# Kernel optimization log

Hardware: AMD Instinct MI355X
Metric: run time of the kernel (lower is better)

Reference implementation:

```python
import jax, jax.numpy as jnp
import numpy as np

B, T, C, H = 4, 4096, 512, 64

def setup_inputs() -> dict:
    key = jax.random.key(0)
    ks = jax.random.split(key, 9)
    k = jax.random.normal(ks[0], (B, T, C), dtype=jnp.float32)
    v = jax.random.normal(ks[1], (B, T, C), dtype=jnp.float32)
    q = jax.random.normal(ks[2], (B, T, C), dtype=jnp.float32)
    # causal lower-triangular mask, positions with 0 are masked to -inf
    mask = jnp.tril(jnp.ones((T, T), dtype=jnp.int32))
    s = 1.0 / np.sqrt(C)
    kW = jax.random.normal(ks[3], (C, H), dtype=jnp.float32) * s
    kb = jax.random.normal(ks[4], (H,), dtype=jnp.float32) * s
    vW = jax.random.normal(ks[5], (C, H), dtype=jnp.float32) * s
    vb = jax.random.normal(ks[6], (H,), dtype=jnp.float32) * s
    qW = jax.random.normal(ks[7], (C, H), dtype=jnp.float32) * s
    qb = jax.random.normal(ks[8], (H,), dtype=jnp.float32) * s
    return {"k": k, "v": v, "q": q, "mask": mask,
            "kW": kW, "kb": kb, "vW": vW, "vb": vb, "qW": qW, "qb": qb}

def reference(k, v, q, mask, kW, kb, vW, vb, qW, qb):
    C_in = k.shape[-1]
    kp = k @ kW + kb                              # [B,T,H]
    qp = q @ qW + qb                              # [B,T,H]
    # NOTE: original scales by embedding_size**-0.5 (C), not head_size**-0.5
    attn = jnp.einsum('bth,bsh->bts', qp, kp) * (C_in ** -0.5)  # [B,T,T]
    attn = jnp.where(mask[None, :, :] == 0, -jnp.inf, attn)
    attn = jax.nn.softmax(attn, axis=-1)
    vp = v @ vW + vb                              # [B,T,H]
    out = attn @ vp                               # [B,T,H]
    return out
```

## Files before the change

kernel.cpp:

```cpp
#include <hip/hip_runtime.h>
#include <hip/hip_bf16.h>

#define Bq 4
#define Tq 4096
#define Cq 512
#define Hq 64
#define NEG_BIG (-3.0e38f)

using bf16   = __bf16;
using bf16x8 = __attribute__((ext_vector_type(8))) __bf16;
using bf16x4 = __attribute__((ext_vector_type(4))) __bf16;
using f32x4  = __attribute__((ext_vector_type(4))) float;
using f32x16 = __attribute__((ext_vector_type(16))) float;

static __device__ __forceinline__ float other_half_f(float x) {
    return __shfl_xor(x, 32, 64);
}
static __device__ __forceinline__ unsigned other_half_u(unsigned x) {
    return (unsigned)__shfl_xor((int)x, 32, 64);
}
static __device__ __forceinline__ unsigned pk2(float x, float y) {
    union { bf16 h[2]; unsigned u; } t;
    t.h[0] = (bf16)x; t.h[1] = (bf16)y;
    return t.u;
}
union W8 { unsigned u[4]; bf16x8 v; };

#define BUILD_B(p, BA, BB) do {                                                \
    const unsigned w0 = pk2(p[0],  p[1]),  w1 = pk2(p[2],  p[3]);              \
    const unsigned w2 = pk2(p[4],  p[5]),  w3 = pk2(p[6],  p[7]);              \
    const unsigned w4 = pk2(p[8],  p[9]),  w5 = pk2(p[10], p[11]);             \
    const unsigned w6 = pk2(p[12], p[13]), w7 = pk2(p[14], p[15]);             \
    const unsigned o0 = other_half_u(w0), o1 = other_half_u(w1);               \
    const unsigned o2 = other_half_u(w2), o3 = other_half_u(w3);               \
    const unsigned o4 = other_half_u(w4), o5 = other_half_u(w5);               \
    const unsigned o6 = other_half_u(w6), o7 = other_half_u(w7);               \
    BA.u[0] = hi ? o2 : w0;  BA.u[1] = hi ? o3 : w1;                           \
    BA.u[2] = hi ? w2 : o0;  BA.u[3] = hi ? w3 : o1;                           \
    BB.u[0] = hi ? o6 : w4;  BB.u[1] = hi ? o7 : w5;                           \
    BB.u[2] = hi ? w6 : o4;  BB.u[3] = hi ? w7 : o5;                           \
} while (0)

__global__ __launch_bounds__(256) void prep_weights_kernel(
    const float* __restrict__ kW, const float* __restrict__ qW,
    const float* __restrict__ vW, bf16* __restrict__ WT)
{
    int i = blockIdx.x * 256 + threadIdx.x;
    int t = i >> 15;
    int r = i & 32767;
    int c = r >> 6;
    int h = r & 63;
    const float* W = (t == 0) ? kW : (t == 1) ? qW : vW;
    WT[(size_t)t * 32768 + h * 512 + c] = (bf16)W[r];
}

__global__ __launch_bounds__(256, 2) void proj_kernel(
    const float* __restrict__ Xk, const float* __restrict__ Xq,
    const float* __restrict__ Xv, const bf16* __restrict__ WT,
    const float* __restrict__ bk, const float* __restrict__ bq,
    const float* __restrict__ bv,
    bf16* __restrict__ kp, bf16* __restrict__ qp, bf16* __restrict__ vpT)
{
    const int t    = blockIdx.y;
    const int lane = threadIdx.x & 63;
    const int wave = threadIdx.x >> 6;
    const int lq   = lane & 15;
    const int lg   = lane >> 4;
    const int row0 = blockIdx.x * 64 + wave * 16;

    const float* X    = (t == 0) ? Xk : (t == 1) ? Xq : Xv;
    const float* bias = (t == 0) ? bk : (t == 1) ? bq : bv;
    const bf16*  Wt   = WT + (size_t)t * (Hq * Cq);

    const float* Xrow = X + (size_t)(row0 + lq) * Cq + lg * 8;

    float4 ra[16], rb[16];
#pragma unroll
    for (int i = 0; i < 16; ++i) {
        ra[i] = *(const float4*)(Xrow + i * 32);
        rb[i] = *(const float4*)(Xrow + i * 32 + 4);
    }
    __builtin_amdgcn_sched_barrier(0);

    f32x4 acc[4];
#pragma unroll
    for (int i = 0; i < 4; ++i) acc[i] = f32x4{0.f, 0.f, 0.f, 0.f};

#pragma unroll
    for (int i = 0; i < 16; ++i) {
        bf16x8 af;
        af[0] = (bf16)ra[i].x; af[1] = (bf16)ra[i].y;
        af[2] = (bf16)ra[i].z; af[3] = (bf16)ra[i].w;
        af[4] = (bf16)rb[i].x; af[5] = (bf16)rb[i].y;
        af[6] = (bf16)rb[i].z; af[7] = (bf16)rb[i].w;
        const int kc = i * 32;
#pragma unroll
        for (int ht = 0; ht < 4; ++ht) {
            bf16x8 bfB = *(const bf16x8*)(Wt + (size_t)(ht * 16 + lq) * Cq + kc + lg * 8);
            acc[ht] = __builtin_amdgcn_mfma_f32_16x16x32_bf16(af, bfB, acc[ht], 0, 0, 0);
        }
    }

    const float scale = (t == 1) ? (0.044194173824159216f * 1.4426950408889634f) : 1.0f;

    if (t < 2) {
        bf16* dst = (t == 0) ? kp : qp;
#pragma unroll
        for (int ht = 0; ht < 4; ++ht) {
            float bb = bias[ht * 16 + lq];
#pragma unroll
            for (int r = 0; r < 4; ++r) {
                int row = row0 + 4 * lg + r;
                dst[(size_t)row * Hq + ht * 16 + lq] = (bf16)((acc[ht][r] + bb) * scale);
            }
        }
    } else {
#pragma unroll
        for (int ht = 0; ht < 4; ++ht) {
            float bb = bias[ht * 16 + lq];
            bf16x4 pk;
#pragma unroll
            for (int r = 0; r < 4; ++r) pk[r] = (bf16)(acc[ht][r] + bb);
            int rowg = row0 + 4 * lg;
            int bidx = rowg >> 12;
            int tt   = rowg & 4095;
            int h    = ht * 16 + lq;
            *(bf16x4*)(vpT + (((size_t)(bidx * Hq + h)) << 12) + tt) = pk;
        }
    }
}

__global__ __launch_bounds__(256, 2) void attn_kernel(
    const bf16* __restrict__ qp, const bf16* __restrict__ kp,
    const bf16* __restrict__ vpT,
    bf16* __restrict__ PO, float* __restrict__ PML)
{
    __shared__ char lds_raw[2][16384];

    const int x = blockIdx.x;
    const int b = x & 3;
    const int j = 31 - ((x >> 2) & 31);
    const int c = x >> 7;
    const int kstart = c * 512;
    const int klim   = (j + 1) * 128;
    if (kstart >= klim) return;
    const int kend = min(kstart + 512, klim);
    const int nt   = (kend - kstart) >> 6;

    const int tid  = threadIdx.x;
    const int wid  = tid >> 6;
    const int lane = tid & 63;
    const int l31  = lane & 31;
    const int half = lane >> 5;
    const bool hi  = half != 0;
    const int qt   = j * 4 + wid;
    const int qb   = qt * 32;
    const int qg   = qb + l31;
    const int qlast = qb + 31;

    const bf16* kp_b = kp  + (size_t)b * Tq * Hq;
    const bf16* vp_b = vpT + (size_t)b * Hq * Tq;

    const int srow = tid >> 2;
    const int sseg = (tid & 3) * 16;
    const int sswz = (srow & 7) << 4;

#define STAGE_LOAD(T, r0, r1, r2, r3) do {                                     \
    const int k0_ = kstart + (T) * 64;                                         \
    const bf16* kg_ = kp_b + (size_t)(k0_ + srow) * Hq + (sseg >> 1);          \
    r0 = *(const int4*)(kg_);                                                  \
    r1 = *(const int4*)(kg_ + 32);                                             \
    const bf16* vg_ = vp_b + (size_t)srow * Tq + k0_ + (sseg >> 1);            \
    r2 = *(const int4*)(vg_);                                                  \
    r3 = *(const int4*)(vg_ + 32);                                             \
} while (0)

#define STAGE_WRITE(BUF, r0, r1, r2, r3) do {                                  \
    char* base_ = lds_raw[BUF];                                                \
    *(int4*)(base_ + srow * 128 + (sseg ^ sswz))          = r0;                \
    *(int4*)(base_ + srow * 128 + ((sseg + 64) ^ sswz))   = r1;                \
    *(int4*)(base_ + 8192 + srow * 128 + (sseg ^ sswz))        = r2;           \
    *(int4*)(base_ + 8192 + srow * 128 + ((sseg + 64) ^ sswz)) = r3;           \
} while (0)

    const bf16* qrow = qp + ((size_t)b * Tq + qb + l31) * Hq + half * 8;
    const bf16x8 Q0 = *(const bf16x8*)(qrow);
    const bf16x8 Q1 = *(const bf16x8*)(qrow + 16);
    const bf16x8 Q2 = *(const bf16x8*)(qrow + 32);
    const bf16x8 Q3 = *(const bf16x8*)(qrow + 48);

    f32x16 O0, O1;
#pragma unroll
    for (int r = 0; r < 16; ++r) { O0[r] = 0.f; O1[r] = 0.f; }
    float l = 0.f;

    const int rswz = (l31 & 7) << 4;
    const int cb   = half * 16;

    int4 s0, s1, s2, s3;
    STAGE_LOAD(0, s0, s1, s2, s3);
    STAGE_WRITE(0, s0, s1, s2, s3);
    __syncthreads();

    int cur = 0;
    for (int t = 0; t < nt; ++t) {
        const bool more = (t + 1 < nt);
        if (more) STAGE_LOAD(t + 1, s0, s1, s2, s3);

        const int k0t = kstart + t * 64;
        if (k0t <= qlast) {
            const char* base = lds_raw[cur];
            const char* kr0 = base + l31 * 128;
            const char* kr1 = base + (32 + l31) * 128;
            const char* vr0 = base + 8192 + l31 * 128;
            const char* vr1 = base + 8192 + (32 + l31) * 128;

            const bf16x8 K00 = *(const bf16x8*)(kr0 + ((cb +  0) ^ rswz));
            const bf16x8 K01 = *(const bf16x8*)(kr0 + ((cb + 32) ^ rswz));
            const bf16x8 K02 = *(const bf16x8*)(kr0 + ((cb + 64) ^ rswz));
            const bf16x8 K03 = *(const bf16x8*)(kr0 + ((cb + 96) ^ rswz));
            const bf16x8 K10 = *(const bf16x8*)(kr1 + ((cb +  0) ^ rswz));
            const bf16x8 K11 = *(const bf16x8*)(kr1 + ((cb + 32) ^ rswz));
            const bf16x8 K12 = *(const bf16x8*)(kr1 + ((cb + 64) ^ rswz));
            const bf16x8 K13 = *(const bf16x8*)(kr1 + ((cb + 96) ^ rswz));
            const bf16x8 Vh0k0 = *(const bf16x8*)(vr0 + ((cb +  0) ^ rswz));
            const bf16x8 Vh0k1 = *(const bf16x8*)(vr0 + ((cb + 32) ^ rswz));
            const bf16x8 Vh0k2 = *(const bf16x8*)(vr0 + ((cb + 64) ^ rswz));
            const bf16x8 Vh0k3 = *(const bf16x8*)(vr0 + ((cb + 96) ^ rswz));
            const bf16x8 Vh1k0 = *(const bf16x8*)(vr1 + ((cb +  0) ^ rswz));
            const bf16x8 Vh1k1 = *(const bf16x8*)(vr1 + ((cb + 32) ^ rswz));
            const bf16x8 Vh1k2 = *(const bf16x8*)(vr1 + ((cb + 64) ^ rswz));
            const bf16x8 Vh1k3 = *(const bf16x8*)(vr1 + ((cb + 96) ^ rswz));

            f32x16 S0, S1;
#pragma unroll
            for (int r = 0; r < 16; ++r) { S0[r] = 0.f; S1[r] = 0.f; }
            S0 = __builtin_amdgcn_mfma_f32_32x32x16_bf16(K00, Q0, S0, 0, 0, 0);
            S1 = __builtin_amdgcn_mfma_f32_32x32x16_bf16(K10, Q0, S1, 0, 0, 0);
            S0 = __builtin_amdgcn_mfma_f32_32x32x16_bf16(K01, Q1, S0, 0, 0, 0);
            S1 = __builtin_amdgcn_mfma_f32_32x32x16_bf16(K11, Q1, S1, 0, 0, 0);
            S0 = __builtin_amdgcn_mfma_f32_32x32x16_bf16(K02, Q2, S0, 0, 0, 0);
            S1 = __builtin_amdgcn_mfma_f32_32x32x16_bf16(K12, Q2, S1, 0, 0, 0);
            S0 = __builtin_amdgcn_mfma_f32_32x32x16_bf16(K03, Q3, S0, 0, 0, 0);
            S1 = __builtin_amdgcn_mfma_f32_32x32x16_bf16(K13, Q3, S1, 0, 0, 0);

            if (k0t + 63 > qb) {
#pragma unroll
                for (int r = 0; r < 16; ++r) {
                    const int kg = k0t + (r & 3) + 8 * (r >> 2) + 4 * half;
                    if (kg > qg)      S0[r] = NEG_BIG;
                    if (kg + 32 > qg) S1[r] = NEG_BIG;
                }
            }

            float p0[16], p1[16];
#pragma unroll
            for (int r = 0; r < 16; ++r) {
                p0[r] = exp2f(S0[r]);
                p1[r] = exp2f(S1[r]);
            }
            l += (((p0[0]+p0[1])+(p0[2]+p0[3])) + ((p0[4]+p0[5])+(p0[6]+p0[7])))
               + (((p0[8]+p0[9])+(p0[10]+p0[11])) + ((p0[12]+p0[13])+(p0[14]+p0[15])))
               + (((p1[0]+p1[1])+(p1[2]+p1[3])) + ((p1[4]+p1[5])+(p1[6]+p1[7])))
               + (((p1[8]+p1[9])+(p1[10]+p1[11])) + ((p1[12]+p1[13])+(p1[14]+p1[15])));

            W8 B00, B01, B10, B11;
            BUILD_B(p0, B00, B01);
            BUILD_B(p1, B10, B11);

            O0 = __builtin_amdgcn_mfma_f32_32x32x16_bf16(Vh0k0, B00.v, O0, 0, 0, 0);
            O1 = __builtin_amdgcn_mfma_f32_32x32x16_bf16(Vh1k0, B00.v, O1, 0, 0, 0);
            O0 = __builtin_amdgcn_mfma_f32_32x32x16_bf16(Vh0k1, B01.v, O0, 0, 0, 0);
            O1 = __builtin_amdgcn_mfma_f32_32x32x16_bf16(Vh1k1, B01.v, O1, 0, 0, 0);
            O0 = __builtin_amdgcn_mfma_f32_32x32x16_bf16(Vh0k2, B10.v, O0, 0, 0, 0);
            O1 = __builtin_amdgcn_mfma_f32_32x32x16_bf16(Vh1k2, B10.v, O1, 0, 0, 0);
            O0 = __builtin_amdgcn_mfma_f32_32x32x16_bf16(Vh0k3, B11.v, O0, 0, 0, 0);
            O1 = __builtin_amdgcn_mfma_f32_32x32x16_bf16(Vh1k3, B11.v, O1, 0, 0, 0);
        }

        __syncthreads();
        if (more) STAGE_WRITE(cur ^ 1, s0, s1, s2, s3);
        __syncthreads();
        cur ^= 1;
    }
#undef STAGE_LOAD
#undef STAGE_WRITE

    const float ltot = l + other_half_f(l);
    const float inv  = (ltot > 0.f) ? (1.0f / ltot) : 0.f;
    const size_t slot = ((size_t)(b * 128 + qt)) * 8 + c;
    bf16* po = PO + slot * 2048;
#pragma unroll
    for (int r = 0; r < 16; ++r) {
        const int h = (r & 3) + 8 * (r >> 2) + 4 * half;
        po[h * 32 + l31]        = (bf16)(O0[r] * inv);
        po[(h + 32) * 32 + l31] = (bf16)(O1[r] * inv);
    }
    if (lane < 32) {
        PML[slot * 32 + l31] = ltot;
    }
}

__global__ __launch_bounds__(256) void combine_kernel(
    const bf16* __restrict__ PO, const float* __restrict__ PML,
    float* __restrict__ out)
{
    const int gid = blockIdx.x;
    const int b   = gid & 3;
    const int qt  = gid >> 2;
    const int qb  = qt * 32;
    const int nch = ((qt >> 2) + 4) >> 2;
    const size_t slot0 = ((size_t)(b * 128 + qt)) * 8;
    const int tid = threadIdx.x;
    const int q   = tid & 31;
    const int hh  = tid >> 5;

    float L = 0.f;
    float acc[8];
#pragma unroll
    for (int i = 0; i < 8; ++i) acc[i] = 0.f;

    for (int c = 0; c < nch; ++c) {
        const float w = PML[(slot0 + c) * 32 + q];
        L += w;
        const bf16* po = PO + (slot0 + c) * 2048;
#pragma unroll
        for (int ih = 0; ih < 8; ++ih)
            acc[ih] += w * (float)po[(hh + 8 * ih) * 32 + q];
    }
    const float inv = 1.0f / L;
#pragma unroll
    for (int ih = 0; ih < 8; ++ih)
        out[((size_t)b * Tq + qb + q) * Hq + hh + 8 * ih] = acc[ih] * inv;
}

extern "C" void kernel_launch(void* const* d_in, const int* in_sizes, int n_in,
                              void* d_out, int out_size, void* d_ws, size_t ws_size,
                              hipStream_t stream)
{
    const float* k  = (const float*)d_in[0];
    const float* v  = (const float*)d_in[1];
    const float* q  = (const float*)d_in[2];
    const float* kW = (const float*)d_in[4];
    const float* kb = (const float*)d_in[5];
    const float* vW = (const float*)d_in[6];
    const float* vb = (const float*)d_in[7];
    const float* qW = (const float*)d_in[8];
    const float* qb = (const float*)d_in[9];
    float* out = (float*)d_out;

    char* ws = (char*)d_ws;
    bf16*  WT  = (bf16*)(ws);
    bf16*  kp  = (bf16*)(ws + 196608);
    bf16*  qp  = (bf16*)(ws + 196608 + 2097152);
    bf16*  vpT = (bf16*)(ws + 196608 + 2 * 2097152);
    bf16*  PO  = (bf16*)(ws + 196608 + 3 * 2097152);
    float* PML = (float*)(ws + 196608 + 3 * 2097152 + 16777216);

    hipLaunchKernelGGL(prep_weights_kernel, dim3(384), dim3(256), 0, stream,
                       kW, qW, vW, WT);
    hipLaunchKernelGGL(proj_kernel, dim3(256, 3), dim3(256), 0, stream,
                       k, q, v, WT, kb, qb, vb, kp, qp, vpT);
    hipLaunchKernelGGL(attn_kernel, dim3(1024), dim3(256), 0, stream,
                       qp, kp, vpT, PO, PML);
    hipLaunchKernelGGL(combine_kernel, dim3(512), dim3(256), 0, stream,
                       PO, PML, out);
}
```

Baseline: 85.75 us.

## Stage projection inputs through double-buffered LDS with async global_load_lds

Result: faster. 82.66 us (-3.6%).

```diff
diff --git a/kernel.cpp b/kernel.cpp
--- a/kernel.cpp
+++ b/kernel.cpp
@@ -61,47 +61,74 @@
     const float* __restrict__ bv,
     bf16* __restrict__ kp, bf16* __restrict__ qp, bf16* __restrict__ vpT)
 {
-    const int t    = blockIdx.y;
-    const int lane = threadIdx.x & 63;
-    const int wave = threadIdx.x >> 6;
-    const int lq   = lane & 15;
-    const int lg   = lane >> 4;
-    const int row0 = blockIdx.x * 64 + wave * 16;
-
+    __shared__ float Xs[2][64 * 128];
+
+    const int t = blockIdx.y;
     const float* X    = (t == 0) ? Xk : (t == 1) ? Xq : Xv;
     const float* bias = (t == 0) ? bk : (t == 1) ? bq : bv;
     const bf16*  Wt   = WT + (size_t)t * (Hq * Cq);
 
-    const float* Xrow = X + (size_t)(row0 + lq) * Cq + lg * 8;
-
-    float4 ra[16], rb[16];
-#pragma unroll
-    for (int i = 0; i < 16; ++i) {
-        ra[i] = *(const float4*)(Xrow + i * 32);
-        rb[i] = *(const float4*)(Xrow + i * 32 + 4);
-    }
-    __builtin_amdgcn_sched_barrier(0);
+    const int tid  = threadIdx.x;
+    const int wave = tid >> 6;
+    const int lane = tid & 63;
+    const int lq   = lane & 15;
+    const int lg   = lane >> 4;
+    const int r0   = blockIdx.x * 64;
+    const float* Xb = X + (size_t)r0 * Cq;
+
+#define STAGE(BUF, STEP) do {                                                  \
+    const int kc_ = (STEP) * 128;                                              \
+    _Pragma("unroll")                                                          \
+    for (int j = 0; j < 8; ++j) {                                              \
+        const int i2   = wave * 8 + j;                                         \
+        const int rloc = 2 * i2 + (lane >> 5);                                 \
+        const int scol = (lane & 31) ^ (rloc & 7);                             \
+        const float* src_ = Xb + (size_t)rloc * Cq + kc_ + scol * 4;           \
+        __builtin_amdgcn_global_load_lds(                                      \
+            (const __attribute__((address_space(1))) void*)(src_),             \
+            (__attribute__((address_space(3))) void*)(&Xs[BUF][i2 * 256]),     \
+            16, 0, 0);                                                         \
+    }                                                                          \
+} while (0)
 
     f32x4 acc[4];
 #pragma unroll
     for (int i = 0; i < 4; ++i) acc[i] = f32x4{0.f, 0.f, 0.f, 0.f};
 
-#pragma unroll
-    for (int i = 0; i < 16; ++i) {
-        bf16x8 af;
-        af[0] = (bf16)ra[i].x; af[1] = (bf16)ra[i].y;
-        af[2] = (bf16)ra[i].z; af[3] = (bf16)ra[i].w;
-        af[4] = (bf16)rb[i].x; af[5] = (bf16)rb[i].y;
-        af[6] = (bf16)rb[i].z; af[7] = (bf16)rb[i].w;
-        const int kc = i * 32;
-#pragma unroll
-        for (int ht = 0; ht < 4; ++ht) {
-            bf16x8 bfB = *(const bf16x8*)(Wt + (size_t)(ht * 16 + lq) * Cq + kc + lg * 8);
-            acc[ht] = __builtin_amdgcn_mfma_f32_16x16x32_bf16(af, bfB, acc[ht], 0, 0, 0);
+    STAGE(0, 0);
+    __syncthreads();
+
+    const int rloc_c = wave * 16 + lq;
+    const int sw     = lq & 7;
+
+#pragma unroll
+    for (int s = 0; s < 4; ++s) {
+        if (s < 3) STAGE((s + 1) & 1, s + 1);
+        const float* lb = &Xs[s & 1][0] + (size_t)rloc_c * 128;
+
+#pragma unroll
+        for (int ch = 0; ch < 4; ++ch) {
+            const int c = ch * 8 + lg * 2;
+            const float4 x0 = *(const float4*)(lb + ((c ^ sw) * 4));
+            const float4 x1 = *(const float4*)(lb + (((c + 1) ^ sw) * 4));
+            bf16x8 af;
+            af[0] = (bf16)x0.x; af[1] = (bf16)x0.y;
+            af[2] = (bf16)x0.z; af[3] = (bf16)x0.w;
+            af[4] = (bf16)x1.x; af[5] = (bf16)x1.y;
+            af[6] = (bf16)x1.z; af[7] = (bf16)x1.w;
+            const int kg = s * 128 + ch * 32;
+#pragma unroll
+            for (int ht = 0; ht < 4; ++ht) {
+                bf16x8 bfB = *(const bf16x8*)(Wt + (size_t)(ht * 16 + lq) * Cq + kg + lg * 8);
+                acc[ht] = __builtin_amdgcn_mfma_f32_16x16x32_bf16(af, bfB, acc[ht], 0, 0, 0);
+            }
         }
-    }
+        __syncthreads();
+    }
+#undef STAGE
 
     const float scale = (t == 1) ? (0.044194173824159216f * 1.4426950408889634f) : 1.0f;
+    const int row0 = r0 + wave * 16;
 
     if (t < 2) {
         bf16* dst = (t == 0) ? kp : qp;
```
